# Optimization experiments

Measured on AMD Instinct MI355X. Metric: run time of the kernel, lower is better.

The kernel has to match this reference:

```python
import jax, jax.numpy as jnp
import numpy as np

B, L, D, H = 8, 1024, 512, 8  # L must equal len_ for the skew trick
DH = D // H


def setup_inputs() -> dict:
    key = jax.random.key(0)
    ks = jax.random.split(key, 6)
    s = 0.02
    return {
        "x": jax.random.normal(ks[0], (B, L, D), dtype=jnp.float32),
        "Wq": jax.random.normal(ks[1], (D, D), dtype=jnp.float32) * s,
        "Wk": jax.random.normal(ks[2], (D, D), dtype=jnp.float32) * s,
        "Wv": jax.random.normal(ks[3], (D, D), dtype=jnp.float32) * s,
        "We": jax.random.normal(ks[4], (L, DH), dtype=jnp.float32) * s,  # e_projection weight: (len_, d_head)
        "Wo": jax.random.normal(ks[5], (D, D), dtype=jnp.float32) * s,
        "bo": jnp.zeros((D,), dtype=jnp.float32),
        "unused": 0,
    }


def reference(x, Wq, Wk, Wv, We, Wo, bo, unused):
    Bx, Lx, Dx = x.shape
    q = (x @ Wq.T).reshape(Bx, Lx, H, DH)  # blhd
    k = (x @ Wk.T).reshape(Bx, Lx, H, DH)
    v = (x @ Wv.T).reshape(Bx, Lx, H, DH)

    # relative-position logits: e_projection(q) then permute -> (B, H, L, len_)
    qe = jnp.einsum('blhd,ed->bhle', q, We)

    # 'skew' trick: reflect-pad right by L-1, zero-pad (right 1, bottom L-1),
    # reshape (B,H,2L-1,2L) -> (B,H,2L,2L-1), slice [:L, L-1:] -> (B,H,L,L)
    qe = jnp.pad(qe, ((0, 0), (0, 0), (0, 0), (0, Lx - 1)), mode='reflect')
    qe = jnp.pad(qe, ((0, 0), (0, 0), (0, Lx - 1), (0, 1)))
    qe = qe.reshape(Bx, H, 2 * Lx, 2 * Lx - 1)
    s_rel = qe[:, :, :Lx, Lx - 1:]

    scale = 1.0 / jnp.sqrt(jnp.asarray(DH, dtype=x.dtype))
    scores = jnp.einsum('blhd,bshd->bhls', q, k)
    A = jax.nn.softmax(scale * (scores + s_rel), axis=-1)
    V = jnp.einsum('bhls,bshd->blhd', A, v).reshape(Bx, Lx, Dx)
    return V @ Wo.T + bo
```

## Files before the change

kernel.cpp:

```cpp
#include <hip/hip_runtime.h>

#define Lc 1024
#define Dc 512
#define Hc 8
#define DHc 64

typedef __attribute__((ext_vector_type(8))) short bf16x8;
typedef __attribute__((ext_vector_type(4))) float f32x4;

typedef __attribute__((address_space(1))) const unsigned int guint;
typedef __attribute__((address_space(3))) unsigned int luint;

__device__ __forceinline__ void gload_lds16(const void* g, void* l) {
    __builtin_amdgcn_global_load_lds((guint*)g, (luint*)l, 16, 0, 0);
}

__device__ __forceinline__ unsigned short f2bf(float f) {
    unsigned u = __float_as_uint(f);
    u += 0x7fffu + ((u >> 16) & 1u);
    return (unsigned short)(u >> 16);
}
__device__ __forceinline__ unsigned short f2bft(float f) {
    return (unsigned short)(__float_as_uint(f) >> 16);
}
__device__ __forceinline__ unsigned pk2(float a, float b) {
    return (unsigned)f2bf(a) | ((unsigned)f2bf(b) << 16);
}
__device__ __forceinline__ float bf2f(unsigned short s) { return __uint_as_float(((unsigned)s) << 16); }

__global__ void cvt_all_kernel(
    const float* __restrict__ x,  const float* __restrict__ Wq,
    const float* __restrict__ Wk, const float* __restrict__ Wv,
    const float* __restrict__ Wo, const float* __restrict__ We,
    unsigned short* __restrict__ xb,  unsigned short* __restrict__ wqb,
    unsigned short* __restrict__ wkb, unsigned short* __restrict__ wvb,
    unsigned short* __restrict__ wob, unsigned short* __restrict__ wet)
{
    int bid = blockIdx.x;
    const float* src; unsigned short* dst; size_t base;
    if      (bid < 4096) { src = x;  dst = xb;  base = (size_t)bid * 1024; }
    else if (bid < 4352) { src = Wq; dst = wqb; base = (size_t)(bid-4096) * 1024; }
    else if (bid < 4608) { src = Wk; dst = wkb; base = (size_t)(bid-4352) * 1024; }
    else if (bid < 4864) { src = Wv; dst = wvb; base = (size_t)(bid-4608) * 1024; }
    else if (bid < 5120) { src = Wo; dst = wob; base = (size_t)(bid-4864) * 1024; }
    else                 { src = We; dst = wet; base = (size_t)(bid-5120) * 1024; }
    size_t i = base + (size_t)threadIdx.x * 4;
    float4 a = *(const float4*)&src[i];
    *(uint2*)&dst[i] = make_uint2(pk2(a.x, a.y), pk2(a.z, a.w));
}

__global__ __launch_bounds__(256, 3) void proj_mfma_kernel(
    const unsigned short* __restrict__ xb,
    const unsigned short* __restrict__ wq, const unsigned short* __restrict__ wk,
    const unsigned short* __restrict__ wv,
    unsigned short* __restrict__ qo, unsigned short* __restrict__ ko,
    unsigned short* __restrict__ vtg, float qscale)
{
    const unsigned short* W;
    if (blockIdx.z == 0)      W = wq;
    else if (blockIdx.z == 1) W = wk;
    else                      W = wv;

    __shared__ unsigned short smem[128 * 136];
    unsigned short* As = smem;
    unsigned short* Bs = smem + 8192;

    const int t = threadIdx.x;
    const int lane = t & 63, w = t >> 6;
    const int lq = lane >> 4, ln = lane & 15;
    const int m0 = blockIdx.y * 128, n0 = blockIdx.x * 128;
    const int wm = (w & 1) * 64, wn = (w >> 1) * 64;
    const int srow = t >> 3;
    const int lsg  = ((t & 7) ^ ((t >> 3) & 7)) * 8;
    const int key  = ln & 7;

    f32x4 acc[4][4];
    #pragma unroll
    for (int i = 0; i < 4; i++)
        #pragma unroll
        for (int j = 0; j < 4; j++) acc[i][j] = (f32x4){0.f,0.f,0.f,0.f};

    for (int c0 = 0; c0 < 512; c0 += 64) {
        __syncthreads();
        #pragma unroll
        for (int g = 0; g < 4; g++) {
            gload_lds16(&xb[(size_t)(m0 + 32*g + srow) * 512 + c0 + lsg], &As[(32*g + srow)*64 + (t&7)*8]);
            gload_lds16(&W [(size_t)(n0 + 32*g + srow) * 512 + c0 + lsg], &Bs[(32*g + srow)*64 + (t&7)*8]);
        }
        __syncthreads();

        #pragma unroll
        for (int kk = 0; kk < 2; kk++) {
            bf16x8 af[4], bf[4];
            #pragma unroll
            for (int i = 0; i < 4; i++)
                af[i] = *(bf16x8*)&As[(wm + 16*i + ln)*64 + ((kk*4 + lq) ^ key)*8];
            #pragma unroll
            for (int j = 0; j < 4; j++)
                bf[j] = *(bf16x8*)&Bs[(wn + 16*j + ln)*64 + ((kk*4 + lq) ^ key)*8];
            #pragma unroll
            for (int i = 0; i < 4; i++)
                #pragma unroll
                for (int j = 0; j < 4; j++)
                    acc[i][j] = __builtin_amdgcn_mfma_f32_16x16x32_bf16(af[i], bf[j], acc[i][j], 0, 0, 0);
        }
    }

    if (blockIdx.z < 2) {
        unsigned short* out = (blockIdx.z == 0) ? qo : ko;
        const float osc = (blockIdx.z == 0) ? qscale : 1.0f;
        #pragma unroll
        for (int i = 0; i < 4; i++) {
            #pragma unroll
            for (int r = 0; r < 4; r++) {
                int m = m0 + wm + 16*i + 4*lq + r;
                int b = m >> 10, l = m & 1023;
                #pragma unroll
                for (int j = 0; j < 4; j++) {
                    int n = n0 + wn + 16*j + ln;
                    int h = n >> 6, dh = n & 63;
                    out[((size_t)((b*Hc + h)*Lc + l))*DHc + dh] = f2bf(acc[i][j][r] * osc);
                }
            }
        }
    } else {
        __syncthreads();
        unsigned short* Ts = smem;
        #pragma unroll
        for (int i = 0; i < 4; i++) {
            int mlb = wm + 16*i + 4*lq;
            #pragma unroll
            for (int j = 0; j < 4; j++) {
                int nl = wn + 16*j + ln;
                *(uint2*)&Ts[nl*136 + mlb] = make_uint2(pk2(acc[i][j][0], acc[i][j][1]),
                                                        pk2(acc[i][j][2], acc[i][j][3]));
            }
        }
        __syncthreads();
        const int b = m0 >> 10, l0m = m0 & 1023;
        const int nl = t >> 1, seg = (t & 1) * 64;
        const int ng = n0 + nl, h = ng >> 6, dh = ng & 63;
        unsigned short* dst = vtg + (((size_t)(b*Hc + h))*DHc + dh)*Lc + l0m + seg;
        #pragma unroll
        for (int u = 0; u < 8; u++)
            *(uint4*)&dst[8*u] = *(uint4*)&Ts[nl*136 + seg + 8*u];
    }
}

__global__ __launch_bounds__(256, 4) void out_mfma_kernel(
    const unsigned short* __restrict__ A, const unsigned short* __restrict__ W,
    const float* __restrict__ bias, float* __restrict__ out)
{
    __shared__ unsigned short As[64 * 64];
    __shared__ unsigned short Bs[64 * 64];

    const int t = threadIdx.x;
    const int lane = t & 63, w = t >> 6;
    const int lq = lane >> 4, ln = lane & 15;
    const int m0 = blockIdx.y * 64, n0 = blockIdx.x * 64;
    const int wm = (w & 1) * 32, wn = (w >> 1) * 32;
    const int srow = t >> 3;
    const int lsg  = ((t & 7) ^ ((t >> 3) & 7)) * 8;
    const int key  = ln & 7;

    f32x4 acc[2][2];
    #pragma unroll
    for (int i = 0; i < 2; i++)
        #pragma unroll
        for (int j = 0; j < 2; j++) acc[i][j] = (f32x4){0.f,0.f,0.f,0.f};

    for (int c0 = 0; c0 < 512; c0 += 64) {
        __syncthreads();
        #pragma unroll
        for (int g = 0; g < 2; g++) {
            gload_lds16(&A[(size_t)(m0 + 32*g + srow) * 512 + c0 + lsg], &As[(32*g + srow)*64 + (t&7)*8]);
            gload_lds16(&W[(size_t)(n0 + 32*g + srow) * 512 + c0 + lsg], &Bs[(32*g + srow)*64 + (t&7)*8]);
        }
        __syncthreads();

        #pragma unroll
        for (int kk = 0; kk < 2; kk++) {
            bf16x8 af[2], bf[2];
            #pragma unroll
            for (int i = 0; i < 2; i++)
                af[i] = *(bf16x8*)&As[(wm + 16*i + ln)*64 + ((kk*4 + lq) ^ key)*8];
            #pragma unroll
            for (int j = 0; j < 2; j++)
                bf[j] = *(bf16x8*)&Bs[(wn + 16*j + ln)*64 + ((kk*4 + lq) ^ key)*8];
            #pragma unroll
            for (int i = 0; i < 2; i++)
                #pragma unroll
                for (int j = 0; j < 2; j++)
                    acc[i][j] = __builtin_amdgcn_mfma_f32_16x16x32_bf16(af[i], bf[j], acc[i][j], 0, 0, 0);
        }
    }

    float bb[2];
    #pragma unroll
    for (int j = 0; j < 2; j++) bb[j] = bias[n0 + wn + 16*j + ln];

    #pragma unroll
    for (int i = 0; i < 2; i++) {
        #pragma unroll
        for (int r = 0; r < 4; r++) {
            int m = m0 + wm + 16*i + 4*lq + r;
            #pragma unroll
            for (int j = 0; j < 2; j++) {
                int n = n0 + wn + 16*j + ln;
                out[(size_t)m * Dc + n] = acc[i][j][r] + bb[j];
            }
        }
    }
}

__global__ __launch_bounds__(256, 4) void attn_v6_kernel(
    const unsigned short* __restrict__ q, const unsigned short* __restrict__ k,
    const unsigned short* __restrict__ vtg, const unsigned short* __restrict__ wet,
    unsigned short* __restrict__ attn)
{
    __shared__ unsigned short ksp [2 * 64 * 32];
    __shared__ unsigned short vtp [2 * 64 * 32];
    __shared__ unsigned short ps  [2 * 64 * 32];
    __shared__ unsigned short qes [128 * 64];

    unsigned short* wesp = ps;

    const int t    = threadIdx.x;
    const int lane = t & 63, w = t >> 6;
    const int lq   = lane >> 4, ln = lane & 15;

    const int n   = blockIdx.x;
    const int xcd = n & 7, idx = n >> 3;
    const int bh  = xcd * 8 + (idx >> 4);
    const int l0  = (idx & 15) * 64;

    const unsigned short* qb  = q   + (size_t)bh * (Lc * DHc);
    const unsigned short* kb  = k   + (size_t)bh * (Lc * DHc);
    const unsigned short* vtb = vtg + (size_t)bh * (DHc * Lc);

    const int trow = t >> 2;
    const int sseg = ((t & 3) ^ ((t >> 4) & 3)) * 8;
    const int swz  = (ln >> 2) & 3;

    const bf16x8 onesf = {(short)0x3F80,(short)0x3F80,(short)0x3F80,(short)0x3F80,
                          (short)0x3F80,(short)0x3F80,(short)0x3F80,(short)0x3F80};

    bf16x8 qa[2];
    #pragma unroll
    for (int kk = 0; kk < 2; kk++)
        qa[kk] = *(const bf16x8*)&qb[(size_t)(l0 + 16*w + ln)*64 + kk*32 + lq*8];

    const int pb0 = 15 - (l0 >> 6);
    gload_lds16(&wet[(size_t)(64*pb0 + trow)*64 +      sseg], &wesp[t*8]);
    gload_lds16(&wet[(size_t)(64*pb0 + trow)*64 + 32 + sseg], &wesp[2048 + t*8]);
    __syncthreads();
    {
        f32x4 qec[4];
        #pragma unroll
        for (int c = 0; c < 4; c++) qec[c] = (f32x4){0.f,0.f,0.f,0.f};
        #pragma unroll
        for (int kk = 0; kk < 2; kk++)
            #pragma unroll
            for (int c = 0; c < 4; c++) {
                bf16x8 bf = *(bf16x8*)&wesp[kk*2048 + (16*c + ln)*32 + (lq ^ swz)*8];
                qec[c] = __builtin_amdgcn_mfma_f32_16x16x32_bf16(qa[kk], bf, qec[c], 0, 0, 0);
            }
        const int cb = (pb0 & 1) * 64;
        #pragma unroll
        for (int c = 0; c < 4; c++) {
            const int row = cb + 16*c + ln;
            *(uint2*)&qes[row*64 + ((16*w + 4*lq) ^ (ln << 2))] =
                make_uint2(pk2(qec[c][0], qec[c][1]), pk2(qec[c][2], qec[c][3]));
        }
    }

    f32x4 Lacc = (f32x4){0.f, 0.f, 0.f, 0.f};
    f32x4 Ov[4];
    #pragma unroll
    for (int c = 0; c < 4; c++) Ov[c] = (f32x4){0.f, 0.f, 0.f, 0.f};

    int pbOld = pb0 - 1;

    for (int s0 = 0; s0 < Lc; s0 += 64) {
        const int c0  = l0 - s0;
        const int ac0 = c0 < 0 ? -c0 : c0;
        const int pb  = (960 - ac0) >> 6;
        const int newp = (pb > pbOld) ? pb + 1 : pb;
        pbOld = pb;
        const int cb = (newp & 1) * 64;

        __syncthreads();
        gload_lds16(&kb [(size_t)(s0 + trow)*64 +      sseg], &ksp [t*8]);
        gload_lds16(&kb [(size_t)(s0 + trow)*64 + 32 + sseg], &ksp [2048 + t*8]);
        gload_lds16(&vtb[(size_t)trow*1024 + s0 +      sseg], &vtp [t*8]);
        gload_lds16(&vtb[(size_t)trow*1024 + s0 + 32 + sseg], &vtp [2048 + t*8]);
        gload_lds16(&wet[(size_t)(64*newp + trow)*64 +      sseg], &wesp[t*8]);
        gload_lds16(&wet[(size_t)(64*newp + trow)*64 + 32 + sseg], &wesp[2048 + t*8]);
        __syncthreads();

        {
            f32x4 qec[4];
            #pragma unroll
            for (int c = 0; c < 4; c++) qec[c] = (f32x4){0.f,0.f,0.f,0.f};
            #pragma unroll
            for (int kk = 0; kk < 2; kk++)
                #pragma unroll
                for (int c = 0; c < 4; c++) {
                    bf16x8 bf = *(bf16x8*)&wesp[kk*2048 + (16*c + ln)*32 + (lq ^ swz)*8];
                    qec[c] = __builtin_amdgcn_mfma_f32_16x16x32_bf16(qa[kk], bf, qec[c], 0, 0, 0);
                }
            #pragma unroll
            for (int c = 0; c < 4; c++) {
                const int row = cb + 16*c + ln;
                *(uint2*)&qes[row*64 + ((16*w + 4*lq) ^ (ln << 2))] =
                    make_uint2(pk2(qec[c][0], qec[c][1]), pk2(qec[c][2], qec[c][3]));
            }
        }

        __syncthreads();

        f32x4 sc[4];
        #pragma unroll
        for (int c = 0; c < 4; c++) sc[c] = (f32x4){0.f,0.f,0.f,0.f};
        #pragma unroll
        for (int kk = 0; kk < 2; kk++)
            #pragma unroll
            for (int c = 0; c < 4; c++) {
                bf16x8 bfk = *(bf16x8*)&ksp[kk*2048 + (16*c + ln)*32 + (lq ^ swz)*8];
                sc[c] = __builtin_amdgcn_mfma_f32_16x16x32_bf16(qa[kk], bfk, sc[c], 0, 0, 0);
            }

        float p[4][4];
        #pragma unroll
        for (int r = 0; r < 4; r++) {
            const int lr = 16*w + 4*lq + r;
            const int dbase = c0 + lr - ln;
            #pragma unroll
            for (int c = 0; c < 4; c++) {
                int d  = dbase - 16*c;
                int ad = d < 0 ? -d : d;
                int m  = 1023 - ad;
                int row = m & 127;
                float bias = bf2f(qes[row*64 + (lr ^ ((m & 15) << 2))]);
                p[r][c] = __builtin_amdgcn_exp2f(sc[c][r] + bias);
            }
        }

        #pragma unroll
        for (int r = 0; r < 4; r++) {
            const int lr = 16*w + 4*lq + r;
            #pragma unroll
            for (int c = 0; c < 4; c++) {
                int seg = (((c & 1)*2 + (ln >> 3)) ^ lq);
                ps[(c >> 1)*2048 + lr*32 + seg*8 + (ln & 7)] = f2bft(p[r][c]);
            }
        }

        #pragma unroll
        for (int kk = 0; kk < 2; kk++) {
            bf16x8 pa = *(bf16x8*)&ps[kk*2048 + (16*w + ln)*32 + (lq ^ swz)*8];
            Lacc = __builtin_amdgcn_mfma_f32_16x16x32_bf16(pa, onesf, Lacc, 0, 0, 0);
            #pragma unroll
            for (int c = 0; c < 4; c++) {
                bf16x8 vf = *(bf16x8*)&vtp[kk*2048 + (16*c + ln)*32 + (lq ^ swz)*8];
                Ov[c] = __builtin_amdgcn_mfma_f32_16x16x32_bf16(pa, vf, Ov[c], 0, 0, 0);
            }
        }
    }

    const int b = bh >> 3, h = bh & 7;
    #pragma unroll
    for (int r = 0; r < 4; r++) {
        float inv = 1.f / Lacc[r];
        int l = l0 + 16*w + 4*lq + r;
        #pragma unroll
        for (int c = 0; c < 4; c++)
            attn[((size_t)(b*Lc + l))*Dc + h*DHc + 16*c + ln] = f2bf(Ov[c][r] * inv);
    }
}

extern "C" void kernel_launch(void* const* d_in, const int* in_sizes, int n_in,
                              void* d_out, int out_size, void* d_ws, size_t ws_size,
                              hipStream_t stream)
{
    (void)in_sizes; (void)n_in; (void)out_size; (void)ws_size;
    const float* x  = (const float*)d_in[0];
    const float* Wq = (const float*)d_in[1];
    const float* Wk = (const float*)d_in[2];
    const float* Wv = (const float*)d_in[3];
    const float* We = (const float*)d_in[4];
    const float* Wo = (const float*)d_in[5];
    const float* bo = (const float*)d_in[6];

    const size_t NT = (size_t)8 * Hc * Lc * DHc;
    unsigned short* qw  = (unsigned short*)d_ws;
    unsigned short* kw  = qw  + NT;
    unsigned short* vtg = kw  + NT;
    unsigned short* xbf = vtg + NT;
    unsigned short* awb = xbf + NT;
    unsigned short* wqb = awb + NT;
    unsigned short* wkb = wqb + 262144;
    unsigned short* wvb = wkb + 262144;
    unsigned short* wob = wvb + 262144;
    unsigned short* wet = wob + 262144;

    cvt_all_kernel<<<5184, 256, 0, stream>>>(x, Wq, Wk, Wv, Wo, We,
                                             xbf, wqb, wkb, wvb, wob, wet);
    proj_mfma_kernel<<<dim3(4, 64, 3), 256, 0, stream>>>(xbf, wqb, wkb, wvb,
                                                         qw, kw, vtg,
                                                         0.125f * 1.44269504089f);
    attn_v6_kernel<<<1024, 256, 0, stream>>>(qw, kw, vtg, wet, awb);
    out_mfma_kernel<<<dim3(8, 128), 256, 0, stream>>>(awb, wob, bo, (float*)d_out);
}
```

Measured before the change: 181.4 us.

## Re-tile attention waves as 2x2 grid sharing B-operand fragments across row groups

Each of the four waves in the attention block now computes a 32-row by 32-column sub-tile (two row groups by two column tiles) instead of 16 rows by all 64 columns. Each LDS fragment of We, K and V is therefore loaded once and reused across two MFMAs, cutting LDS read traffic per MFMA. The catch is that the P tile is now produced and consumed by different waves, so an extra __syncthreads per iteration is added before the PV product. Each wave also holds twice as many Q fragments.

```diff
diff --git a/kernel.cpp b/kernel.cpp
--- a/kernel.cpp
+++ b/kernel.cpp
@@ -213,7 +213,7 @@
     }
 }
 
-__global__ __launch_bounds__(256, 4) void attn_v6_kernel(
+__global__ __launch_bounds__(256, 4) void attn_v7_kernel(
     const unsigned short* __restrict__ q, const unsigned short* __restrict__ k,
     const unsigned short* __restrict__ vtg, const unsigned short* __restrict__ wet,
     unsigned short* __restrict__ attn)
@@ -228,6 +228,8 @@
     const int t    = threadIdx.x;
     const int lane = t & 63, w = t >> 6;
     const int lq   = lane >> 4, ln = lane & 15;
+    const int wr   = (w >> 1) * 32;
+    const int wc   = w & 1;
 
     const int n   = blockIdx.x;
     const int xcd = n & 7, idx = n >> 3;
@@ -245,39 +247,52 @@
     const bf16x8 onesf = {(short)0x3F80,(short)0x3F80,(short)0x3F80,(short)0x3F80,
                           (short)0x3F80,(short)0x3F80,(short)0x3F80,(short)0x3F80};
 
-    bf16x8 qa[2];
-    #pragma unroll
-    for (int kk = 0; kk < 2; kk++)
-        qa[kk] = *(const bf16x8*)&qb[(size_t)(l0 + 16*w + ln)*64 + kk*32 + lq*8];
+    bf16x8 qa[2][2];
+    #pragma unroll
+    for (int rg = 0; rg < 2; rg++)
+        #pragma unroll
+        for (int kk = 0; kk < 2; kk++)
+            qa[rg][kk] = *(const bf16x8*)&qb[(size_t)(l0 + wr + 16*rg + ln)*64 + kk*32 + lq*8];
 
     const int pb0 = 15 - (l0 >> 6);
     gload_lds16(&wet[(size_t)(64*pb0 + trow)*64 +      sseg], &wesp[t*8]);
     gload_lds16(&wet[(size_t)(64*pb0 + trow)*64 + 32 + sseg], &wesp[2048 + t*8]);
     __syncthreads();
     {
-        f32x4 qec[4];
-        #pragma unroll
-        for (int c = 0; c < 4; c++) qec[c] = (f32x4){0.f,0.f,0.f,0.f};
+        f32x4 qec[2][2];
+        #pragma unroll
+        for (int rg = 0; rg < 2; rg++)
+            #pragma unroll
+            for (int ct = 0; ct < 2; ct++) qec[rg][ct] = (f32x4){0.f,0.f,0.f,0.f};
         #pragma unroll
         for (int kk = 0; kk < 2; kk++)
             #pragma unroll
-            for (int c = 0; c < 4; c++) {
-                bf16x8 bf = *(bf16x8*)&wesp[kk*2048 + (16*c + ln)*32 + (lq ^ swz)*8];
-                qec[c] = __builtin_amdgcn_mfma_f32_16x16x32_bf16(qa[kk], bf, qec[c], 0, 0, 0);
+            for (int ct = 0; ct < 2; ct++) {
+                bf16x8 bf = *(bf16x8*)&wesp[kk*2048 + (16*(2*wc+ct) + ln)*32 + (lq ^ swz)*8];
+                #pragma unroll
+                for (int rg = 0; rg < 2; rg++)
+                    qec[rg][ct] = __builtin_amdgcn_mfma_f32_16x16x32_bf16(qa[rg][kk], bf, qec[rg][ct], 0, 0, 0);
             }
         const int cb = (pb0 & 1) * 64;
         #pragma unroll
-        for (int c = 0; c < 4; c++) {
-            const int row = cb + 16*c + ln;
-            *(uint2*)&qes[row*64 + ((16*w + 4*lq) ^ (ln << 2))] =
-                make_uint2(pk2(qec[c][0], qec[c][1]), pk2(qec[c][2], qec[c][3]));
-        }
-    }
-
-    f32x4 Lacc = (f32x4){0.f, 0.f, 0.f, 0.f};
-    f32x4 Ov[4];
-    #pragma unroll
-    for (int c = 0; c < 4; c++) Ov[c] = (f32x4){0.f, 0.f, 0.f, 0.f};
+        for (int ct = 0; ct < 2; ct++) {
+            const int row = cb + 16*(2*wc+ct) + ln;
+            #pragma unroll
+            for (int rg = 0; rg < 2; rg++)
+                *(uint2*)&qes[row*64 + ((wr + 16*rg + 4*lq) ^ (ln << 2))] =
+                    make_uint2(pk2(qec[rg][ct][0], qec[rg][ct][1]),
+                               pk2(qec[rg][ct][2], qec[rg][ct][3]));
+        }
+    }
+
+    f32x4 Lacc[2];
+    f32x4 Ov[2][2];
+    #pragma unroll
+    for (int rg = 0; rg < 2; rg++) {
+        Lacc[rg] = (f32x4){0.f,0.f,0.f,0.f};
+        #pragma unroll
+        for (int ct = 0; ct < 2; ct++) Ov[rg][ct] = (f32x4){0.f,0.f,0.f,0.f};
+    }
 
     int pbOld = pb0 - 1;
 
@@ -299,84 +314,98 @@
         __syncthreads();
 
         {
-            f32x4 qec[4];
-            #pragma unroll
-            for (int c = 0; c < 4; c++) qec[c] = (f32x4){0.f,0.f,0.f,0.f};
+            f32x4 qec[2][2];
+            #pragma unroll
+            for (int rg = 0; rg < 2; rg++)
+                #pragma unroll
+                for (int ct = 0; ct < 2; ct++) qec[rg][ct] = (f32x4){0.f,0.f,0.f,0.f};
             #pragma unroll
             for (int kk = 0; kk < 2; kk++)
                 #pragma unroll
-                for (int c = 0; c < 4; c++) {
-                    bf16x8 bf = *(bf16x8*)&wesp[kk*2048 + (16*c + ln)*32 + (lq ^ swz)*8];
-                    qec[c] = __builtin_amdgcn_mfma_f32_16x16x32_bf16(qa[kk], bf, qec[c], 0, 0, 0);
+                for (int ct = 0; ct < 2; ct++) {
+                    bf16x8 bf = *(bf16x8*)&wesp[kk*2048 + (16*(2*wc+ct) + ln)*32 + (lq ^ swz)*8];
+                    #pragma unroll
+                    for (int rg = 0; rg < 2; rg++)
+                        qec[rg][ct] = __builtin_amdgcn_mfma_f32_16x16x32_bf16(qa[rg][kk], bf, qec[rg][ct], 0, 0, 0);
                 }
             #pragma unroll
-            for (int c = 0; c < 4; c++) {
-                const int row = cb + 16*c + ln;
-                *(uint2*)&qes[row*64 + ((16*w + 4*lq) ^ (ln << 2))] =
-                    make_uint2(pk2(qec[c][0], qec[c][1]), pk2(qec[c][2], qec[c][3]));
-            }
-        }
-
-        __syncthreads();
-
-        f32x4 sc[4];
-        #pragma unroll
-        for (int c = 0; c < 4; c++) sc[c] = (f32x4){0.f,0.f,0.f,0.f};
+            for (int ct = 0; ct < 2; ct++) {
+                const int row = cb + 16*(2*wc+ct) + ln;
+                #pragma unroll
+                for (int rg = 0; rg < 2; rg++)
+                    *(uint2*)&qes[row*64 + ((wr + 16*rg + 4*lq) ^ (ln << 2))] =
+                        make_uint2(pk2(qec[rg][ct][0], qec[rg][ct][1]),
+                                   pk2(qec[rg][ct][2], qec[rg][ct][3]));
+            }
+        }
+
+        __syncthreads();
+
+        f32x4 sc[2][2];
+        #pragma unroll
+        for (int rg = 0; rg < 2; rg++)
+            #pragma unroll
+            for (int ct = 0; ct < 2; ct++) sc[rg][ct] = (f32x4){0.f,0.f,0.f,0.f};
         #pragma unroll
         for (int kk = 0; kk < 2; kk++)
             #pragma unroll
-            for (int c = 0; c < 4; c++) {
-                bf16x8 bfk = *(bf16x8*)&ksp[kk*2048 + (16*c + ln)*32 + (lq ^ swz)*8];
-                sc[c] = __builtin_amdgcn_mfma_f32_16x16x32_bf16(qa[kk], bfk, sc[c], 0, 0, 0);
-            }
-
-        float p[4][4];
+            for (int ct = 0; ct < 2; ct++) {
+                bf16x8 bfk = *(bf16x8*)&ksp[kk*2048 + (16*(2*wc+ct) + ln)*32 + (lq ^ swz)*8];
+                #pragma unroll
+                for (int rg = 0; rg < 2; rg++)
+                    sc[rg][ct] = __builtin_amdgcn_mfma_f32_16x16x32_bf16(qa[rg][kk], bfk, sc[rg][ct], 0, 0, 0);
+            }
+
+        #pragma unroll
+        for (int rg = 0; rg < 2; rg++)
+            #pragma unroll
+            for (int r = 0; r < 4; r++) {
+                const int lr = wr + 16*rg + 4*lq + r;
+                const int dbase = c0 + lr - ln;
+                #pragma unroll
+                for (int ct = 0; ct < 2; ct++) {
+                    int d  = dbase - 16*(2*wc+ct);
+                    int ad = d < 0 ? -d : d;
+                    int m  = 1023 - ad;
+                    float bias = bf2f(qes[(m & 127)*64 + (lr ^ ((m & 15) << 2))]);
+                    float pv = __builtin_amdgcn_exp2f(sc[rg][ct][r] + bias);
+                    int seg = ((ct*2 + (ln >> 3)) ^ lq);
+                    ps[wc*2048 + lr*32 + seg*8 + (ln & 7)] = f2bft(pv);
+                }
+            }
+
+        __syncthreads();
+
+        #pragma unroll
+        for (int kk = 0; kk < 2; kk++) {
+            bf16x8 pa[2];
+            #pragma unroll
+            for (int rg = 0; rg < 2; rg++)
+                pa[rg] = *(bf16x8*)&ps[kk*2048 + (wr + 16*rg + ln)*32 + (lq ^ swz)*8];
+            #pragma unroll
+            for (int rg = 0; rg < 2; rg++)
+                Lacc[rg] = __builtin_amdgcn_mfma_f32_16x16x32_bf16(pa[rg], onesf, Lacc[rg], 0, 0, 0);
+            #pragma unroll
+            for (int ct = 0; ct < 2; ct++) {
+                bf16x8 vf = *(bf16x8*)&vtp[kk*2048 + (16*(2*wc+ct) + ln)*32 + (lq ^ swz)*8];
+                #pragma unroll
+                for (int rg = 0; rg < 2; rg++)
+                    Ov[rg][ct] = __builtin_amdgcn_mfma_f32_16x16x32_bf16(pa[rg], vf, Ov[rg][ct], 0, 0, 0);
+            }
+        }
+    }
+
+    const int b = bh >> 3, h = bh & 7;
+    #pragma unroll
+    for (int rg = 0; rg < 2; rg++)
         #pragma unroll
         for (int r = 0; r < 4; r++) {
-            const int lr = 16*w + 4*lq + r;
-            const int dbase = c0 + lr - ln;
-            #pragma unroll
-            for (int c = 0; c < 4; c++) {
-                int d  = dbase - 16*c;
-                int ad = d < 0 ? -d : d;
-                int m  = 1023 - ad;
-                int row = m & 127;
-                float bias = bf2f(qes[row*64 + (lr ^ ((m & 15) << 2))]);
-                p[r][c] = __builtin_amdgcn_exp2f(sc[c][r] + bias);
-            }
-        }
-
-        #pragma unroll
-        for (int r = 0; r < 4; r++) {
-            const int lr = 16*w + 4*lq + r;
-            #pragma unroll
-            for (int c = 0; c < 4; c++) {
-                int seg = (((c & 1)*2 + (ln >> 3)) ^ lq);
-                ps[(c >> 1)*2048 + lr*32 + seg*8 + (ln & 7)] = f2bft(p[r][c]);
-            }
-        }
-
-        #pragma unroll
-        for (int kk = 0; kk < 2; kk++) {
-            bf16x8 pa = *(bf16x8*)&ps[kk*2048 + (16*w + ln)*32 + (lq ^ swz)*8];
-            Lacc = __builtin_amdgcn_mfma_f32_16x16x32_bf16(pa, onesf, Lacc, 0, 0, 0);
-            #pragma unroll
-            for (int c = 0; c < 4; c++) {
-                bf16x8 vf = *(bf16x8*)&vtp[kk*2048 + (16*c + ln)*32 + (lq ^ swz)*8];
-                Ov[c] = __builtin_amdgcn_mfma_f32_16x16x32_bf16(pa, vf, Ov[c], 0, 0, 0);
-            }
-        }
-    }
-
-    const int b = bh >> 3, h = bh & 7;
-    #pragma unroll
-    for (int r = 0; r < 4; r++) {
-        float inv = 1.f / Lacc[r];
-        int l = l0 + 16*w + 4*lq + r;
-        #pragma unroll
-        for (int c = 0; c < 4; c++)
-            attn[((size_t)(b*Lc + l))*Dc + h*DHc + 16*c + ln] = f2bf(Ov[c][r] * inv);
-    }
+            float inv = 1.f / Lacc[rg][r];
+            int l = l0 + wr + 16*rg + 4*lq + r;
+            #pragma unroll
+            for (int ct = 0; ct < 2; ct++)
+                attn[((size_t)(b*Lc + l))*Dc + h*DHc + 16*(2*wc+ct) + ln] = f2bf(Ov[rg][ct][r] * inv);
+        }
 }
 
 extern "C" void kernel_launch(void* const* d_in, const int* in_sizes, int n_in,
@@ -409,6 +438,6 @@
     proj_mfma_kernel<<<dim3(4, 64, 3), 256, 0, stream>>>(xbf, wqb, wkb, wvb,
                                                          qw, kw, vtg,
                                                          0.125f * 1.44269504089f);
-    attn_v6_kernel<<<1024, 256, 0, stream>>>(qw, kw, vtg, wet, awb);
+    attn_v7_kernel<<<1024, 256, 0, stream>>>(qw, kw, vtg, wet, awb);
     out_mfma_kernel<<<dim3(8, 128), 256, 0, stream>>>(awb, wob, bo, (float*)d_out);
 }
```

After: 173.8 us. -4.2%, faster.

## Rework attention kernel to 32x32 MFMA tiles with register-resident P and split-S warps

Applied to the files above, without the earlier changes.

Rewrites the attention kernel to use 32x32x16 bf16 MFMA instead of 16x16x32. The four waves are split two along query rows and two along key positions. Scores are computed transposed so the probabilities can be repacked into MFMA operands in registers via permlane32 swaps, removing the LDS round trip for P. Row sums become scalar register adds instead of a ones-matrix MFMA. K and We tile loads are prefetched one stage ahead, and the two key-split halves are reduced through shared memory at the end. This adds complexity, a final cross-wave reduction, and a larger LDS footprint.

```diff
diff --git a/kernel.cpp b/kernel.cpp
--- a/kernel.cpp
+++ b/kernel.cpp
@@ -7,6 +7,7 @@
 
 typedef __attribute__((ext_vector_type(8))) short bf16x8;
 typedef __attribute__((ext_vector_type(4))) float f32x4;
+typedef __attribute__((ext_vector_type(16))) float f32x16;
 
 typedef __attribute__((address_space(1))) const unsigned int guint;
 typedef __attribute__((address_space(3))) unsigned int luint;
@@ -20,13 +21,17 @@
     u += 0x7fffu + ((u >> 16) & 1u);
     return (unsigned short)(u >> 16);
 }
-__device__ __forceinline__ unsigned short f2bft(float f) {
-    return (unsigned short)(__float_as_uint(f) >> 16);
-}
 __device__ __forceinline__ unsigned pk2(float a, float b) {
     return (unsigned)f2bf(a) | ((unsigned)f2bf(b) << 16);
 }
+__device__ __forceinline__ unsigned pk2t(float a, float b) {
+    return __builtin_amdgcn_perm(__float_as_uint(b), __float_as_uint(a), 0x07060302u);
+}
 __device__ __forceinline__ float bf2f(unsigned short s) { return __uint_as_float(((unsigned)s) << 16); }
+
+__device__ __forceinline__ void pl32swap(unsigned &a, unsigned &b) {
+    asm volatile("v_permlane32_swap_b32 %0, %1" : "+v"(a), "+v"(b));
+}
 
 __global__ void cvt_all_kernel(
     const float* __restrict__ x,  const float* __restrict__ Wq,
@@ -213,21 +218,22 @@
     }
 }
 
-__global__ __launch_bounds__(256, 4) void attn_v6_kernel(
+__global__ __launch_bounds__(256, 4) void attn_v12_kernel(
     const unsigned short* __restrict__ q, const unsigned short* __restrict__ k,
     const unsigned short* __restrict__ vtg, const unsigned short* __restrict__ wet,
     unsigned short* __restrict__ attn)
 {
-    __shared__ unsigned short ksp [2 * 64 * 32];
-    __shared__ unsigned short vtp [2 * 64 * 32];
-    __shared__ unsigned short ps  [2 * 64 * 32];
-    __shared__ unsigned short qes [128 * 64];
-
-    unsigned short* wesp = ps;
+    __shared__ unsigned short smem[20480];
+    unsigned short* ksp  = smem;
+    unsigned short* vtp  = smem + 4096;
+    unsigned short* wesp = smem + 8192;
+    unsigned short* qes  = smem + 12288;
 
     const int t    = threadIdx.x;
     const int lane = t & 63, w = t >> 6;
-    const int lq   = lane >> 4, ln = lane & 15;
+    const int ln31 = lane & 31, hi = lane >> 5;
+    const int si   = w >> 1;
+    const int li   = w & 1;
 
     const int n   = blockIdx.x;
     const int xcd = n & 7, idx = n >> 3;
@@ -238,49 +244,51 @@
     const unsigned short* kb  = k   + (size_t)bh * (Lc * DHc);
     const unsigned short* vtb = vtg + (size_t)bh * (DHc * Lc);
 
-    const int trow = t >> 2;
-    const int sseg = ((t & 3) ^ ((t >> 4) & 3)) * 8;
-    const int swz  = (ln >> 2) & 3;
-
-    const bf16x8 onesf = {(short)0x3F80,(short)0x3F80,(short)0x3F80,(short)0x3F80,
-                          (short)0x3F80,(short)0x3F80,(short)0x3F80,(short)0x3F80};
-
-    bf16x8 qa[2];
-    #pragma unroll
-    for (int kk = 0; kk < 2; kk++)
-        qa[kk] = *(const bf16x8*)&qb[(size_t)(l0 + 16*w + ln)*64 + kk*32 + lq*8];
+    const int srow2 = t >> 3;
+    const int lsg2  = ((t & 7) ^ ((t >> 3) & 7)) * 8;
+    const int k7    = ln31 & 7;
+    const int lloc  = 32*li + ln31;
+
+    bf16x8 qf[4];
+    #pragma unroll
+    for (int kk = 0; kk < 4; kk++)
+        qf[kk] = *(const bf16x8*)&qb[(size_t)(l0 + lloc)*64 + kk*16 + hi*8];
 
     const int pb0 = 15 - (l0 >> 6);
-    gload_lds16(&wet[(size_t)(64*pb0 + trow)*64 +      sseg], &wesp[t*8]);
-    gload_lds16(&wet[(size_t)(64*pb0 + trow)*64 + 32 + sseg], &wesp[2048 + t*8]);
+
+    gload_lds16(&wet[(size_t)(64*pb0 + srow2)*64 + lsg2],        &vtp [t*8]);
+    gload_lds16(&wet[(size_t)(64*pb0 + 32 + srow2)*64 + lsg2],   &vtp [2048 + t*8]);
+    gload_lds16(&wet[(size_t)(64*(pb0+1) + srow2)*64 + lsg2],    &wesp[t*8]);
+    gload_lds16(&wet[(size_t)(64*(pb0+1) + 32 + srow2)*64 + lsg2], &wesp[2048 + t*8]);
+    gload_lds16(&kb [(size_t)srow2*64 + lsg2],                   &ksp [t*8]);
+    gload_lds16(&kb [(size_t)(32 + srow2)*64 + lsg2],            &ksp [2048 + t*8]);
     __syncthreads();
+
     {
-        f32x4 qec[4];
-        #pragma unroll
-        for (int c = 0; c < 4; c++) qec[c] = (f32x4){0.f,0.f,0.f,0.f};
-        #pragma unroll
-        for (int kk = 0; kk < 2; kk++)
-            #pragma unroll
-            for (int c = 0; c < 4; c++) {
-                bf16x8 bf = *(bf16x8*)&wesp[kk*2048 + (16*c + ln)*32 + (lq ^ swz)*8];
-                qec[c] = __builtin_amdgcn_mfma_f32_16x16x32_bf16(qa[kk], bf, qec[c], 0, 0, 0);
-            }
-        const int cb = (pb0 & 1) * 64;
-        #pragma unroll
-        for (int c = 0; c < 4; c++) {
-            const int row = cb + 16*c + ln;
-            *(uint2*)&qes[row*64 + ((16*w + 4*lq) ^ (ln << 2))] =
-                make_uint2(pk2(qec[c][0], qec[c][1]), pk2(qec[c][2], qec[c][3]));
-        }
-    }
-
-    f32x4 Lacc = (f32x4){0.f, 0.f, 0.f, 0.f};
-    f32x4 Ov[4];
-    #pragma unroll
-    for (int c = 0; c < 4; c++) Ov[c] = (f32x4){0.f, 0.f, 0.f, 0.f};
+        f32x16 qec = (f32x16){0.f,0.f,0.f,0.f,0.f,0.f,0.f,0.f,0.f,0.f,0.f,0.f,0.f,0.f,0.f,0.f};
+        #pragma unroll
+        for (int kk = 0; kk < 4; kk++) {
+            bf16x8 wf = *(bf16x8*)&vtp[(32*si + ln31)*64 + ((2*kk + hi) ^ k7)*8];
+            qec = __builtin_amdgcn_mfma_f32_32x32x16_bf16(qf[kk], wf, qec, 0, 0, 0);
+        }
+        const int rs = ((pb0 & 1)*64 + 32*si + ln31) * 64;
+        #pragma unroll
+        for (int g = 0; g < 4; g++) {
+            const int col = (32*li + 8*g + 4*hi) ^ ((ln31 & 15) << 2);
+            *(uint2*)&qes[rs + col] = make_uint2(pk2(qec[4*g], qec[4*g+1]),
+                                                 pk2(qec[4*g+2], qec[4*g+3]));
+        }
+    }
+
+    f32x16 Ov[2];
+    #pragma unroll
+    for (int dt = 0; dt < 2; dt++)
+        Ov[dt] = (f32x16){0.f,0.f,0.f,0.f,0.f,0.f,0.f,0.f,0.f,0.f,0.f,0.f,0.f,0.f,0.f,0.f};
+    float Lacc = 0.f;
 
     int pbOld = pb0 - 1;
 
+    #pragma unroll 1
     for (int s0 = 0; s0 < Lc; s0 += 64) {
         const int c0  = l0 - s0;
         const int ac0 = c0 < 0 ? -c0 : c0;
@@ -288,94 +296,129 @@
         const int newp = (pb > pbOld) ? pb + 1 : pb;
         pbOld = pb;
         const int cb = (newp & 1) * 64;
-
-        __syncthreads();
-        gload_lds16(&kb [(size_t)(s0 + trow)*64 +      sseg], &ksp [t*8]);
-        gload_lds16(&kb [(size_t)(s0 + trow)*64 + 32 + sseg], &ksp [2048 + t*8]);
-        gload_lds16(&vtb[(size_t)trow*1024 + s0 +      sseg], &vtp [t*8]);
-        gload_lds16(&vtb[(size_t)trow*1024 + s0 + 32 + sseg], &vtp [2048 + t*8]);
-        gload_lds16(&wet[(size_t)(64*newp + trow)*64 +      sseg], &wesp[t*8]);
-        gload_lds16(&wet[(size_t)(64*newp + trow)*64 + 32 + sseg], &wesp[2048 + t*8]);
-        __syncthreads();
+        const bool more = (s0 < Lc - 64);
+        const int nc  = c0 - 64;
+        const int nac = nc < 0 ? -nc : nc;
+        const int npb = (960 - nac) >> 6;
+        const int nnp = (npb > pb) ? npb + 1 : npb;
+
+        __syncthreads();
+
+        gload_lds16(&vtb[(size_t)srow2*1024 + s0 + lsg2],        &vtp[t*8]);
+        gload_lds16(&vtb[(size_t)(32 + srow2)*1024 + s0 + lsg2], &vtp[2048 + t*8]);
 
         {
-            f32x4 qec[4];
-            #pragma unroll
-            for (int c = 0; c < 4; c++) qec[c] = (f32x4){0.f,0.f,0.f,0.f};
-            #pragma unroll
-            for (int kk = 0; kk < 2; kk++)
-                #pragma unroll
-                for (int c = 0; c < 4; c++) {
-                    bf16x8 bf = *(bf16x8*)&wesp[kk*2048 + (16*c + ln)*32 + (lq ^ swz)*8];
-                    qec[c] = __builtin_amdgcn_mfma_f32_16x16x32_bf16(qa[kk], bf, qec[c], 0, 0, 0);
-                }
-            #pragma unroll
-            for (int c = 0; c < 4; c++) {
-                const int row = cb + 16*c + ln;
-                *(uint2*)&qes[row*64 + ((16*w + 4*lq) ^ (ln << 2))] =
-                    make_uint2(pk2(qec[c][0], qec[c][1]), pk2(qec[c][2], qec[c][3]));
-            }
-        }
-
-        __syncthreads();
-
-        f32x4 sc[4];
-        #pragma unroll
-        for (int c = 0; c < 4; c++) sc[c] = (f32x4){0.f,0.f,0.f,0.f};
-        #pragma unroll
-        for (int kk = 0; kk < 2; kk++)
-            #pragma unroll
-            for (int c = 0; c < 4; c++) {
-                bf16x8 bfk = *(bf16x8*)&ksp[kk*2048 + (16*c + ln)*32 + (lq ^ swz)*8];
-                sc[c] = __builtin_amdgcn_mfma_f32_16x16x32_bf16(qa[kk], bfk, sc[c], 0, 0, 0);
-            }
-
-        float p[4][4];
-        #pragma unroll
-        for (int r = 0; r < 4; r++) {
-            const int lr = 16*w + 4*lq + r;
-            const int dbase = c0 + lr - ln;
-            #pragma unroll
-            for (int c = 0; c < 4; c++) {
-                int d  = dbase - 16*c;
+            f32x16 qec = (f32x16){0.f,0.f,0.f,0.f,0.f,0.f,0.f,0.f,0.f,0.f,0.f,0.f,0.f,0.f,0.f,0.f};
+            #pragma unroll
+            for (int kk = 0; kk < 4; kk++) {
+                bf16x8 wf = *(bf16x8*)&wesp[(32*si + ln31)*64 + ((2*kk + hi) ^ k7)*8];
+                qec = __builtin_amdgcn_mfma_f32_32x32x16_bf16(qf[kk], wf, qec, 0, 0, 0);
+            }
+            const int rs = (cb + 32*si + ln31) * 64;
+            #pragma unroll
+            for (int g = 0; g < 4; g++) {
+                const int col = (32*li + 8*g + 4*hi) ^ ((ln31 & 15) << 2);
+                *(uint2*)&qes[rs + col] = make_uint2(pk2(qec[4*g], qec[4*g+1]),
+                                                     pk2(qec[4*g+2], qec[4*g+3]));
+            }
+        }
+
+        __syncthreads();
+
+        if (more) {
+            gload_lds16(&wet[(size_t)(64*nnp + srow2)*64 + lsg2],      &wesp[t*8]);
+            gload_lds16(&wet[(size_t)(64*nnp + 32 + srow2)*64 + lsg2], &wesp[2048 + t*8]);
+        }
+
+        f32x16 sc = (f32x16){0.f,0.f,0.f,0.f,0.f,0.f,0.f,0.f,0.f,0.f,0.f,0.f,0.f,0.f,0.f,0.f};
+        #pragma unroll
+        for (int kk = 0; kk < 4; kk++) {
+            bf16x8 kf = *(bf16x8*)&ksp[(32*si + ln31)*64 + ((2*kk + hi) ^ k7)*8];
+            sc = __builtin_amdgcn_mfma_f32_32x32x16_bf16(kf, qf[kk], sc, 0, 0, 0);
+        }
+
+        float p[16];
+        #pragma unroll
+        for (int g = 0; g < 4; g++) {
+            const int sb = 32*si + 8*g + 4*hi;
+            #pragma unroll
+            for (int r = 0; r < 4; r++) {
+                int d  = c0 + lloc - sb - r;
                 int ad = d < 0 ? -d : d;
                 int m  = 1023 - ad;
-                int row = m & 127;
-                float bias = bf2f(qes[row*64 + (lr ^ ((m & 15) << 2))]);
-                p[r][c] = __builtin_amdgcn_exp2f(sc[c][r] + bias);
-            }
-        }
-
-        #pragma unroll
-        for (int r = 0; r < 4; r++) {
-            const int lr = 16*w + 4*lq + r;
-            #pragma unroll
-            for (int c = 0; c < 4; c++) {
-                int seg = (((c & 1)*2 + (ln >> 3)) ^ lq);
-                ps[(c >> 1)*2048 + lr*32 + seg*8 + (ln & 7)] = f2bft(p[r][c]);
-            }
-        }
-
+                float bias = bf2f(qes[(m & 127)*64 + (lloc ^ ((m & 15) << 2))]);
+                p[4*g + r] = __builtin_amdgcn_exp2f(sc[4*g + r] + bias);
+            }
+        }
+        {
+            float t0 = (p[0]+p[1]) + (p[2]+p[3]);
+            float t1 = (p[4]+p[5]) + (p[6]+p[7]);
+            float t2 = (p[8]+p[9]) + (p[10]+p[11]);
+            float t3 = (p[12]+p[13]) + (p[14]+p[15]);
+            Lacc += (t0 + t1) + (t2 + t3);
+        }
+        unsigned d0[4], d1[4];
+        #pragma unroll
+        for (int g = 0; g < 4; g++) {
+            d0[g] = pk2t(p[4*g],     p[4*g + 1]);
+            d1[g] = pk2t(p[4*g + 2], p[4*g + 3]);
+        }
+        bf16x8 pfr[2];
         #pragma unroll
         for (int kk = 0; kk < 2; kk++) {
-            bf16x8 pa = *(bf16x8*)&ps[kk*2048 + (16*w + ln)*32 + (lq ^ swz)*8];
-            Lacc = __builtin_amdgcn_mfma_f32_16x16x32_bf16(pa, onesf, Lacc, 0, 0, 0);
-            #pragma unroll
-            for (int c = 0; c < 4; c++) {
-                bf16x8 vf = *(bf16x8*)&vtp[kk*2048 + (16*c + ln)*32 + (lq ^ swz)*8];
-                Ov[c] = __builtin_amdgcn_mfma_f32_16x16x32_bf16(pa, vf, Ov[c], 0, 0, 0);
-            }
-        }
-    }
-
-    const int b = bh >> 3, h = bh & 7;
-    #pragma unroll
-    for (int r = 0; r < 4; r++) {
-        float inv = 1.f / Lacc[r];
-        int l = l0 + 16*w + 4*lq + r;
-        #pragma unroll
-        for (int c = 0; c < 4; c++)
-            attn[((size_t)(b*Lc + l))*Dc + h*DHc + 16*c + ln] = f2bf(Ov[c][r] * inv);
+            pl32swap(d0[2*kk], d0[2*kk + 1]);
+            pl32swap(d1[2*kk], d1[2*kk + 1]);
+            uint4 fu = make_uint4(d0[2*kk], d1[2*kk], d0[2*kk + 1], d1[2*kk + 1]);
+            pfr[kk] = *(bf16x8*)&fu;
+        }
+
+        __syncthreads();
+
+        if (more) {
+            gload_lds16(&kb[(size_t)(s0 + 64 + srow2)*64 + lsg2],      &ksp[t*8]);
+            gload_lds16(&kb[(size_t)(s0 + 64 + 32 + srow2)*64 + lsg2], &ksp[2048 + t*8]);
+        }
+
+        #pragma unroll
+        for (int kk = 0; kk < 2; kk++)
+            #pragma unroll
+            for (int dt = 0; dt < 2; dt++) {
+                bf16x8 vf = *(bf16x8*)&vtp[(32*dt + ln31)*64 + (((4*si + 2*kk + hi) ^ k7))*8];
+                Ov[dt] = __builtin_amdgcn_mfma_f32_32x32x16_bf16(vf, pfr[kk], Ov[dt], 0, 0, 0);
+            }
+    }
+
+    unsigned la = __float_as_uint(Lacc), lb = la;
+    pl32swap(la, lb);
+    float Lh = Lacc + __uint_as_float(hi ? la : lb);
+
+    __syncthreads();
+    float* scr = (float*)smem;
+    if (si == 1) {
+        #pragma unroll
+        for (int dt = 0; dt < 2; dt++)
+            #pragma unroll
+            for (int rg = 0; rg < 16; rg++)
+                scr[(dt*16 + rg)*128 + li*64 + lane] = Ov[dt][rg];
+        scr[32*128 + li*64 + lane] = Lh;
+    }
+    __syncthreads();
+    if (si == 0) {
+        const float Lt = Lh + scr[32*128 + li*64 + lane];
+        const float inv = 1.f / Lt;
+        const int b = bh >> 3, h = bh & 7;
+        const int lg = l0 + lloc;
+        unsigned short* dst = attn + ((size_t)(b*Lc + lg))*Dc + h*DHc;
+        #pragma unroll
+        for (int dt = 0; dt < 2; dt++)
+            #pragma unroll
+            for (int g = 0; g < 4; g++) {
+                float v0 = (Ov[dt][4*g]   + scr[(dt*16 + 4*g)*128 + li*64 + lane]) * inv;
+                float v1 = (Ov[dt][4*g+1] + scr[(dt*16 + 4*g+1)*128 + li*64 + lane]) * inv;
+                float v2 = (Ov[dt][4*g+2] + scr[(dt*16 + 4*g+2)*128 + li*64 + lane]) * inv;
+                float v3 = (Ov[dt][4*g+3] + scr[(dt*16 + 4*g+3)*128 + li*64 + lane]) * inv;
+                *(uint2*)&dst[32*dt + 8*g + 4*hi] = make_uint2(pk2(v0, v1), pk2(v2, v3));
+            }
     }
 }
 
@@ -409,6 +452,6 @@
     proj_mfma_kernel<<<dim3(4, 64, 3), 256, 0, stream>>>(xbf, wqb, wkb, wvb,
                                                          qw, kw, vtg,
                                                          0.125f * 1.44269504089f);
-    attn_v6_kernel<<<1024, 256, 0, stream>>>(qw, kw, vtg, wet, awb);
+    attn_v12_kernel<<<1024, 256, 0, stream>>>(qw, kw, vtg, wet, awb);
     out_mfma_kernel<<<dim3(8, 128), 256, 0, stream>>>(awb, wob, bo, (float*)d_out);
 }
```

New measurement: 167.2 us. 1.09x faster.
